# Performance work log

Measured on AMD Instinct MI355X. Metric: run time of the kernel, lower is better.

## Reference

```python
import jax, jax.numpy as jnp
import numpy as np

MARGIN = 0.1
PERM_SEED = 42  # fixed stand-in for torch.randperm per row


def setup_inputs() -> dict:
    key = jax.random.key(0)
    k1, k2, k3 = jax.random.split(key, 3)
    n, d, f = 32768, 1000, 300
    inputs = jax.random.normal(k1, (n, f), dtype=jnp.float32)
    Y = jax.random.normal(k2, (d, f), dtype=jnp.float32)
    y_idxs = jax.random.randint(k3, (n,), 0, d)
    return {"inputs": inputs, "Y": Y, "y_idxs": y_idxs}


def reference(inputs, Y, y_idxs):
    # inputs: [n, f], Y: [d, f] class semantic embeddings, y_idxs: [n]
    n, d = inputs.shape[0], Y.shape[0]

    # All dot products at once: S[i, j] = Y[j] . inputs[i]
    S = inputs @ Y.T  # [n, d]

    # One random class permutation per row (torch.randperm(d) per sample)
    perm_keys = jax.random.split(jax.random.key(PERM_SEED), n)
    perms = jax.vmap(lambda k: jax.random.permutation(k, d))(perm_keys)  # [n, d]

    ap = S[jnp.arange(n), y_idxs]                 # [n]   anchor-positive dots
    an = jnp.take_along_axis(S, perms, axis=1)    # [n, d] anchor-negative dots in perm order

    valid = perms != y_idxs[:, None]              # skip j == y
    # early-break condition at each permutation slot
    cond = valid & ((ap[:, None] - an) > MARGIN)
    c = cond.astype(jnp.int32)
    excl_cum = jnp.cumsum(c, axis=1) - c          # exclusive cumsum of break events
    # include every valid slot up to AND including the first breaking slot
    include = valid & (excl_cum == 0)             # [n, d]

    # MarginRankingLoss with target=1: mean(max(0, margin + an - ap))
    per_pair = jnp.maximum(0.0, MARGIN + an - ap[:, None])
    total = jnp.sum(jnp.where(include, per_pair, 0.0))
    count = jnp.maximum(jnp.sum(include), 1).astype(jnp.float32)
    return total / count
```

## Files before the change

kernel.cpp:

```cpp
#include <hip/hip_runtime.h>
#include <stdint.h>

#define N_ROWS 32768
#define D_CLS  1000
#define D_PAD  1024
#define F_DIM  300
#define F_PAD  320
#define MARGIN 0.1f

#define BM     128
#define BN     128
#define BK     64
#define GTHR   512
#define KGTHR  1024
#define LDTA   328
#define LDTB   72

#define M_PB   32
#define NTHR   512
#define NT_PW  8
#define MT_PB  2
#define LDA    328
#define SROW   34

#define NPART  32

typedef short short8 __attribute__((ext_vector_type(8)));
typedef float f32x4  __attribute__((ext_vector_type(4)));

__device__ __forceinline__ uint32_t rotl32(uint32_t x, int r) {
  return (x << r) | (x >> (32 - r));
}

__device__ __forceinline__ void threefry2x32(uint32_t k0, uint32_t k1,
                                             uint32_t x0, uint32_t x1,
                                             uint32_t& o0, uint32_t& o1) {
  uint32_t k2 = k0 ^ k1 ^ 0x1BD11BDAu;
  x0 += k0; x1 += k1;
#define TF_R(r) { x0 += x1; x1 = rotl32(x1, (r)); x1 ^= x0; }
  TF_R(13) TF_R(15) TF_R(26) TF_R(6)
  x0 += k1; x1 += k2 + 1u;
  TF_R(17) TF_R(29) TF_R(16) TF_R(24)
  x0 += k2; x1 += k0 + 2u;
  TF_R(13) TF_R(15) TF_R(26) TF_R(6)
  x0 += k0; x1 += k1 + 3u;
  TF_R(17) TF_R(29) TF_R(16) TF_R(24)
  x0 += k1; x1 += k2 + 4u;
  TF_R(13) TF_R(15) TF_R(26) TF_R(6)
  x0 += k2; x1 += k0 + 5u;
#undef TF_R
  o0 = x0; o1 = x1;
}

struct TFSched {
  uint32_t k0, k1, k2, k2p1, k0p2, k1p3, k2p4, k0p5;
};
__device__ __forceinline__ TFSched tf_make(uint32_t k0, uint32_t k1) {
  TFSched s;
  s.k0 = k0; s.k1 = k1;
  s.k2 = k0 ^ k1 ^ 0x1BD11BDAu;
  s.k2p1 = s.k2 + 1u; s.k0p2 = k0 + 2u; s.k1p3 = k1 + 3u;
  s.k2p4 = s.k2 + 4u; s.k0p5 = k0 + 5u;
  return s;
}
__device__ __forceinline__ uint32_t tf_hash(const TFSched& s, uint32_t c) {
  uint32_t x0 = s.k0, x1 = c + s.k1;
#define TFH(r) { x0 += x1; x1 = __builtin_amdgcn_alignbit(x1, x1, 32 - (r)); x1 ^= x0; }
  TFH(13) TFH(15) TFH(26) TFH(6)
  x0 += s.k1; x1 += s.k2p1;
  TFH(17) TFH(29) TFH(16) TFH(24)
  x0 += s.k2; x1 += s.k0p2;
  TFH(13) TFH(15) TFH(26) TFH(6)
  x0 += s.k0; x1 += s.k1p3;
  TFH(17) TFH(29) TFH(16) TFH(24)
  x0 += s.k1; x1 += s.k2p4;
  TFH(13) TFH(15) TFH(26) TFH(6)
  x0 += s.k2; x1 += s.k0p5;
#undef TFH
  return x0 ^ x1;
}

__device__ __forceinline__ uint16_t f2bf(float f) {
  uint32_t u = __builtin_bit_cast(uint32_t, f);
  return (uint16_t)((u + 0x7FFFu + ((u >> 16) & 1u)) >> 16);
}
__device__ __forceinline__ float bf2f(uint16_t v) {
  return __builtin_bit_cast(float, (uint32_t)v << 16);
}
__device__ __forceinline__ float bf2f_lo(uint32_t v) {
  return __builtin_bit_cast(float, v << 16);
}
__device__ __forceinline__ float bf2f_hi(uint32_t v) {
  return __builtin_bit_cast(float, v & 0xFFFF0000u);
}

__global__ void prep(const float* __restrict__ Y, uint16_t* __restrict__ Ybf,
                     uint32_t* __restrict__ subk) {
  int i = blockIdx.x * 256 + threadIdx.x;
  if (i < D_PAD * F_PAD) {
    int j = i / F_PAD;
    int k = i - j * F_PAD;
    float v = (j < D_CLS && k < F_DIM) ? Y[j * F_DIM + k] : 0.f;
    Ybf[i] = f2bf(v);
  }
  if (i < N_ROWS) {
    uint32_t r1, r2, s1, s2;
    threefry2x32(0u, 42u, 0u, (uint32_t)i, r1, r2);
    threefry2x32(r1, r2, 0u, 1u, s1, s2);
    subk[2 * i]     = s1;
    subk[2 * i + 1] = s2;
  }
}

__launch_bounds__(KGTHR, 4)
__global__ void gemm_kg(const float* __restrict__ inputs,
                        const uint16_t* __restrict__ Ybf,
                        uint32_t* __restrict__ Spair,
                        uint32_t* __restrict__ keyP,
                        const uint32_t* __restrict__ subk) {
  __shared__ __align__(16) uint16_t A_lds[BM * LDTA];
  __shared__ __align__(16) uint16_t B_lds[2][BN * LDTB];

  const int t    = threadIdx.x;
  const int wave = t >> 6;
  const int lane = t & 63;
  const int l15  = lane & 15;
  const int g    = lane >> 4;
  const bool isg = wave < 8;
  const int wm   = wave >> 1;
  const int wn   = wave & 1;
  const int kw   = wave - 8;
  const int r0   = blockIdx.x * BM;

  for (int i = t; i < BM * (F_DIM / 4); i += KGTHR) {
    int r  = i / 75;
    int c4 = i - r * 75;
    float4 v = *(const float4*)(inputs + (size_t)(r0 + r) * F_DIM + c4 * 4);
    ushort4 o;
    o.x = f2bf(v.x); o.y = f2bf(v.y); o.z = f2bf(v.z); o.w = f2bf(v.w);
    *(ushort4*)&A_lds[r * LDTA + c4 * 4] = o;
  }
  for (int i = t; i < BM * 7; i += KGTHR) {
    int r = i / 7, p = i - r * 7;
    *(ushort4*)&A_lds[r * LDTA + 300 + p * 4] = (ushort4){0, 0, 0, 0};
  }

  const int brow = t >> 3, bkof = t & 7;
  short8 bv[2];
  auto LOADB = [&](int tile) {
    const int c0 = (tile / 5) * BN;
    const int k0 = (tile % 5) * BK;
#pragma unroll
    for (int j = 0; j < 2; ++j)
      bv[j] = *(const short8*)(Ybf + (size_t)(c0 + j * 64 + brow) * F_PAD + k0 + bkof * 8);
  };
  auto WRITEB = [&](int buf) {
#pragma unroll
    for (int j = 0; j < 2; ++j)
      *(short8*)&B_lds[buf][(j * 64 + brow) * LDTB + bkof * 8] = bv[j];
  };

  f32x4 acc[2][4];
#pragma unroll
  for (int mt = 0; mt < 2; ++mt)
#pragma unroll
    for (int nt = 0; nt < 4; ++nt) acc[mt][nt] = (f32x4){0.f, 0.f, 0.f, 0.f};

  if (isg) LOADB(0);
  __syncthreads();
  if (isg) WRITEB(0);
  __syncthreads();

  const int NT = 8 * 5;
#pragma unroll 1
  for (int tile = 0; tile < NT; ++tile) {
    if (isg) {
      const int kt = tile % 5;
      if (tile < NT - 1) LOADB(tile + 1);
      const uint16_t* Bc = B_lds[tile & 1];
#pragma unroll
      for (int ks = 0; ks < 2; ++ks) {
        short8 a[2], b[4];
#pragma unroll
        for (int mt = 0; mt < 2; ++mt)
          a[mt] = *(const short8*)&A_lds[(wm * 32 + mt * 16 + l15) * LDTA + kt * BK + ks * 32 + g * 8];
#pragma unroll
        for (int nt = 0; nt < 4; ++nt)
          b[nt] = *(const short8*)&Bc[(wn * 64 + nt * 16 + l15) * LDTB + ks * 32 + g * 8];
#pragma unroll
        for (int mt = 0; mt < 2; ++mt)
#pragma unroll
          for (int nt = 0; nt < 4; ++nt)
            acc[mt][nt] = __builtin_amdgcn_mfma_f32_16x16x32_bf16(a[mt], b[nt], acc[mt][nt], 0, 0, 0);
      }
      if (kt == 4) {
        const int c0 = (tile / 5) * BN;
#pragma unroll
        for (int mt = 0; mt < 2; ++mt)
#pragma unroll
          for (int nt = 0; nt < 4; ++nt) {
            const int col = c0 + wn * 64 + nt * 16 + l15;
#pragma unroll
            for (int p = 0; p < 2; ++p) {
              uint32_t lo = f2bf(acc[mt][nt][2 * p]);
              uint32_t hi = f2bf(acc[mt][nt][2 * p + 1]);
              size_t rp = (size_t)(r0 >> 1) + wm * 16 + mt * 8 + g * 2 + p;
              Spair[rp * D_PAD + col] = (hi << 16) | lo;
            }
            acc[mt][nt] = (f32x4){0.f, 0.f, 0.f, 0.f};
          }
      }
      if (tile < NT - 1) WRITEB((tile + 1) & 1);
    } else if (tile < 32) {
      const int rp_loc = kw * 8 + (tile >> 2);
      const size_t rpg = (size_t)(r0 >> 1) + rp_loc;
      const int rA = r0 + 2 * rp_loc;
      const uint4 sk4 = *(const uint4*)(subk + 2 * rA);
      const TFSched sA = tf_make(sk4.x, sk4.y);
      const TFSched sB = tf_make(sk4.z, sk4.w);
      const uint32_t c0 = (uint32_t)((tile & 3) * 256 + 4 * lane);
      uint4 ov;
      uint32_t o[4];
#pragma unroll
      for (int j = 0; j < 4; ++j) {
        uint32_t kA = tf_hash(sA, c0 + (uint32_t)j);
        uint32_t kB = tf_hash(sB, c0 + (uint32_t)j);
        o[j] = (kA >> 16) | (kB & 0xFFFF0000u);
      }
      ov.x = o[0]; ov.y = o[1]; ov.z = o[2]; ov.w = o[3];
      *(uint4*)(keyP + (rpg << 10) + c0) = ov;
    }
    if (tile < NT - 1) __syncthreads();
  }
}

__launch_bounds__(256, 4)
__global__ void loss_light(const uint32_t* __restrict__ Spair,
                           const uint32_t* __restrict__ keyP,
                           const int* __restrict__ yidx,
                           float* __restrict__ rowSum,
                           int* __restrict__ rowCnt) {
  const int lane = threadIdx.x & 63;
  const int wave = threadIdx.x >> 6;
  const int rp   = blockIdx.x * 4 + wave;
  const int rA   = 2 * rp;
  const int rB   = rA + 1;
  const int yA = yidx[rA], yB = yidx[rB];
  const uint32_t* Sp = Spair + (size_t)rp * D_PAD;
  const uint32_t* Kp = keyP  + (size_t)rp * D_PAD;
  const float apA = bf2f_lo(Sp[yA]);
  const float apB = bf2f_hi(Sp[yB]);

  uint32_t an[16], kk[16];
#pragma unroll
  for (int q4 = 0; q4 < 4; ++q4) {
    uint4 v = *(const uint4*)(Sp + q4 * 256 + lane * 4);
    an[4 * q4 + 0] = v.x; an[4 * q4 + 1] = v.y;
    an[4 * q4 + 2] = v.z; an[4 * q4 + 3] = v.w;
    uint4 w = *(const uint4*)(Kp + q4 * 256 + lane * 4);
    kk[4 * q4 + 0] = w.x; kk[4 * q4 + 1] = w.y;
    kk[4 * q4 + 2] = w.z; kk[4 * q4 + 3] = w.w;
  }

  uint32_t mnA = 0xFFFFu, mnB = 0xFFFFu;
#pragma unroll
  for (int q = 0; q < 16; ++q) {
    const int c = (q >> 2) * 256 + lane * 4 + (q & 3);
    const uint32_t kA = kk[q] & 0xFFFFu, kB = kk[q] >> 16;
    const float anA = bf2f_lo(an[q]), anB = bf2f_hi(an[q]);
    if ((c < D_CLS) && (c != yA) && (apA - anA) > MARGIN) mnA = (kA < mnA) ? kA : mnA;
    if ((c < D_CLS) && (c != yB) && (apB - anB) > MARGIN) mnB = (kB < mnB) ? kB : mnB;
  }
#pragma unroll
  for (int off = 1; off < 64; off <<= 1) {
    uint32_t oA = __shfl_xor(mnA, off, 64);
    uint32_t oB = __shfl_xor(mnB, off, 64);
    mnA = (oA < mnA) ? oA : mnA;
    mnB = (oB < mnB) ? oB : mnB;
  }

  float smA = 0.f, smB = 0.f; int ctA = 0, ctB = 0;
#pragma unroll
  for (int q = 0; q < 16; ++q) {
    const int c = (q >> 2) * 256 + lane * 4 + (q & 3);
    const uint32_t kA = kk[q] & 0xFFFFu, kB = kk[q] >> 16;
    const float anA = bf2f_lo(an[q]), anB = bf2f_hi(an[q]);
    if ((c < D_CLS) && (c != yA) && kA < mnA) { smA += MARGIN + anA - apA; ctA += 1; }
    if ((c < D_CLS) && (c != yB) && kB < mnB) { smB += MARGIN + anB - apB; ctB += 1; }
  }
#pragma unroll
  for (int off = 1; off < 64; off <<= 1) {
    smA += __shfl_xor(smA, off, 64);
    smB += __shfl_xor(smB, off, 64);
    ctA += __shfl_xor(ctA, off, 64);
    ctB += __shfl_xor(ctB, off, 64);
  }
  if (lane == 0) {
    rowSum[rA] = smA;  rowCnt[rA] = ctA + (mnA != 0xFFFFu ? 1 : 0);
    rowSum[rB] = smB;  rowCnt[rB] = ctB + (mnB != 0xFFFFu ? 1 : 0);
  }
}

__launch_bounds__(GTHR, 1)
__global__ void gemm_s(const float* __restrict__ inputs,
                       const uint16_t* __restrict__ Ybf,
                       uint32_t* __restrict__ Spair) {
  __shared__ __align__(16) uint16_t A_lds[BM * LDTA];
  __shared__ __align__(16) uint16_t B_lds[2][BN * LDTB];

  const int t    = threadIdx.x;
  const int wave = t >> 6;
  const int lane = t & 63;
  const int l15  = lane & 15;
  const int g    = lane >> 4;
  const int wm   = wave >> 1;
  const int wn   = wave & 1;
  const int r0   = blockIdx.x * BM;

  for (int i = t; i < BM * (F_DIM / 4); i += GTHR) {
    int r  = i / 75;
    int c4 = i - r * 75;
    float4 v = *(const float4*)(inputs + (size_t)(r0 + r) * F_DIM + c4 * 4);
    ushort4 o;
    o.x = f2bf(v.x); o.y = f2bf(v.y); o.z = f2bf(v.z); o.w = f2bf(v.w);
    *(ushort4*)&A_lds[r * LDTA + c4 * 4] = o;
  }
  for (int i = t; i < BM * 7; i += GTHR) {
    int r = i / 7, p = i - r * 7;
    *(ushort4*)&A_lds[r * LDTA + 300 + p * 4] = (ushort4){0, 0, 0, 0};
  }

  const int brow = t >> 3, bkof = t & 7;
  short8 bv[2];
  auto LOADB = [&](int tile) {
    const int c0 = (tile / 5) * BN;
    const int k0 = (tile % 5) * BK;
#pragma unroll
    for (int j = 0; j < 2; ++j)
      bv[j] = *(const short8*)(Ybf + (size_t)(c0 + j * 64 + brow) * F_PAD + k0 + bkof * 8);
  };
  auto WRITEB = [&](int buf) {
#pragma unroll
    for (int j = 0; j < 2; ++j)
      *(short8*)&B_lds[buf][(j * 64 + brow) * LDTB + bkof * 8] = bv[j];
  };

  f32x4 acc[2][4];
#pragma unroll
  for (int mt = 0; mt < 2; ++mt)
#pragma unroll
    for (int nt = 0; nt < 4; ++nt) acc[mt][nt] = (f32x4){0.f, 0.f, 0.f, 0.f};

  LOADB(0);
  __syncthreads();
  WRITEB(0);
  __syncthreads();

  const int NT = 8 * 5;
#pragma unroll 1
  for (int tile = 0; tile < NT; ++tile) {
    const int kt = tile % 5;
    if (tile < NT - 1) LOADB(tile + 1);
    const uint16_t* Bc = B_lds[tile & 1];
#pragma unroll
    for (int ks = 0; ks < 2; ++ks) {
      short8 a[2], b[4];
#pragma unroll
      for (int mt = 0; mt < 2; ++mt)
        a[mt] = *(const short8*)&A_lds[(wm * 32 + mt * 16 + l15) * LDTA + kt * BK + ks * 32 + g * 8];
#pragma unroll
      for (int nt = 0; nt < 4; ++nt)
        b[nt] = *(const short8*)&Bc[(wn * 64 + nt * 16 + l15) * LDTB + ks * 32 + g * 8];
#pragma unroll
      for (int mt = 0; mt < 2; ++mt)
#pragma unroll
        for (int nt = 0; nt < 4; ++nt)
          acc[mt][nt] = __builtin_amdgcn_mfma_f32_16x16x32_bf16(a[mt], b[nt], acc[mt][nt], 0, 0, 0);
    }
    if (kt == 4) {
      const int c0 = (tile / 5) * BN;
#pragma unroll
      for (int mt = 0; mt < 2; ++mt)
#pragma unroll
        for (int nt = 0; nt < 4; ++nt) {
          const int col = c0 + wn * 64 + nt * 16 + l15;
#pragma unroll
          for (int p = 0; p < 2; ++p) {
            uint32_t lo = f2bf(acc[mt][nt][2 * p]);
            uint32_t hi = f2bf(acc[mt][nt][2 * p + 1]);
            size_t rp = (size_t)(r0 >> 1) + wm * 16 + mt * 8 + g * 2 + p;
            Spair[rp * D_PAD + col] = (hi << 16) | lo;
          }
          acc[mt][nt] = (f32x4){0.f, 0.f, 0.f, 0.f};
        }
    }
    if (tile < NT - 1) {
      WRITEB((tile + 1) & 1);
      __syncthreads();
    }
  }
}

__launch_bounds__(256, 2)
__global__ void hash_loss(const uint32_t* __restrict__ Spair,
                          const uint32_t* __restrict__ subk,
                          const int* __restrict__ yidx,
                          float* __restrict__ rowSum,
                          int* __restrict__ rowCnt) {
  const int lane = threadIdx.x & 63;
  const int wave = threadIdx.x >> 6;
  const int rp   = blockIdx.x * 4 + wave;
  const int rA   = 2 * rp;
  const int rB   = 2 * rp + 1;

  const int yA = yidx[rA], yB = yidx[rB];
  const TFSched sA = tf_make(subk[2 * rA], subk[2 * rA + 1]);
  const TFSched sB = tf_make(subk[2 * rB], subk[2 * rB + 1]);

  const uint32_t* Sp = Spair + (size_t)rp * D_PAD;
  const float apA = bf2f_lo(Sp[yA]);
  const float apB = bf2f_hi(Sp[yB]);

  uint32_t an[16];
#pragma unroll
  for (int j = 0; j < 4; ++j) {
    uint4 v = *(const uint4*)(Sp + j * 256 + lane * 4);
    an[4 * j + 0] = v.x; an[4 * j + 1] = v.y;
    an[4 * j + 2] = v.z; an[4 * j + 3] = v.w;
  }

  uint32_t skAB[16];
  uint32_t pkA = 0xFFFFFFFFu, pkB = 0xFFFFFFFFu;
#pragma unroll
  for (int q = 0; q < 16; ++q) {
    const int c = (q >> 2) * 256 + lane * 4 + (q & 3);
    uint32_t kA = tf_hash(sA, (uint32_t)c);
    uint32_t kB = tf_hash(sB, (uint32_t)c);
    skAB[q] = (kA >> 16) | (kB & 0xFFFF0000u);
    float anA = bf2f_lo(an[q]);
    float anB = bf2f_hi(an[q]);
    if ((c < D_CLS) && (c != yA) && (apA - anA) > MARGIN) {
      pkA = (kA < pkA) ? kA : pkA;
    }
    if ((c < D_CLS) && (c != yB) && (apB - anB) > MARGIN) {
      pkB = (kB < pkB) ? kB : pkB;
    }
  }
#pragma unroll
  for (int off = 1; off < 64; off <<= 1) {
    uint32_t oA = __shfl_xor(pkA, off, 64);
    uint32_t oB = __shfl_xor(pkB, off, 64);
    pkA = (oA < pkA) ? oA : pkA;
    pkB = (oB < pkB) ? oB : pkB;
  }
  const uint32_t pA16 = pkA >> 16;
  const uint32_t pB16 = pkB >> 16;

  float smA = 0.f, smB = 0.f; int ctA = 0, ctB = 0;
#pragma unroll
  for (int q = 0; q < 16; ++q) {
    const int c = (q >> 2) * 256 + lane * 4 + (q & 3);
    float anA = bf2f_lo(an[q]);
    float anB = bf2f_hi(an[q]);
    if ((c < D_CLS) && (c != yA) && (skAB[q] & 0xFFFFu) < pA16) {
      smA += MARGIN + anA - apA; ctA += 1;
    }
    if ((c < D_CLS) && (c != yB) && (skAB[q] >> 16) < pB16) {
      smB += MARGIN + anB - apB; ctB += 1;
    }
  }
#pragma unroll
  for (int off = 1; off < 64; off <<= 1) {
    smA += __shfl_xor(smA, off, 64);
    smB += __shfl_xor(smB, off, 64);
    ctA += __shfl_xor(ctA, off, 64);
    ctB += __shfl_xor(ctB, off, 64);
  }
  if (lane == 0) {
    rowSum[rA] = smA;
    rowCnt[rA] = ctA + (pkA != 0xFFFFFFFFu ? 1 : 0);
    rowSum[rB] = smB;
    rowCnt[rB] = ctB + (pkB != 0xFFFFFFFFu ? 1 : 0);
  }
}

__launch_bounds__(NTHR, 4)
__global__ void triplet_fused(const float* __restrict__ inputs,
                              const uint16_t* __restrict__ Ybf,
                              const int* __restrict__ yidx,
                              float* __restrict__ rowSum,
                              int* __restrict__ rowCnt) {
  __shared__ __align__(16) uint16_t SH[D_PAD * SROW];
  __shared__ int      y_sh[M_PB];
  __shared__ uint32_t subk_sh[M_PB][2];

  const int t    = threadIdx.x;
  const int wave = t >> 6;
  const int lane = t & 63;
  const int l15  = lane & 15;
  const int g    = lane >> 4;
  const int row0 = blockIdx.x * M_PB;
  const int colbase = wave * (NT_PW * 16);

  if (t < M_PB) {
    y_sh[t] = yidx[row0 + t];
    uint32_t r1, r2, s1, s2;
    threefry2x32(0u, 42u, 0u, (uint32_t)(row0 + t), r1, r2);
    threefry2x32(r1, r2, 0u, 1u, s1, s2);
    subk_sh[t][0] = s1; subk_sh[t][1] = s2;
  }

  uint16_t* A_fl = SH;
  for (int i = t; i < M_PB * (F_DIM / 4); i += NTHR) {
    int r  = i / 75;
    int c4 = i - r * 75;
    float4 v = *(const float4*)(inputs + (size_t)(row0 + r) * F_DIM + c4 * 4);
    ushort4 o;
    o.x = f2bf(v.x); o.y = f2bf(v.y); o.z = f2bf(v.z); o.w = f2bf(v.w);
    *(ushort4*)&A_fl[r * LDA + c4 * 4] = o;
  }
  for (int i = t; i < M_PB * 5; i += NTHR) {
    int r = i / 5, p = i - r * 5;
    *(ushort4*)&A_fl[r * LDA + 300 + p * 4] = (ushort4){0, 0, 0, 0};
  }
  __syncthreads();

  f32x4 acc[MT_PB][NT_PW];
#pragma unroll
  for (int mt = 0; mt < MT_PB; ++mt)
#pragma unroll
    for (int nt = 0; nt < NT_PW; ++nt) acc[mt][nt] = (f32x4){0.f, 0.f, 0.f, 0.f};

  const uint16_t* gB[NT_PW];
#pragma unroll
  for (int nt = 0; nt < NT_PW; ++nt) {
    int j = colbase + nt * 16 + l15;
    gB[nt] = Ybf + (size_t)j * F_PAD + (g << 3);
  }
  const uint16_t* aBase = &A_fl[l15 * LDA + (g << 3)];

#pragma unroll 2
  for (int ks = 0; ks < F_PAD / 32; ++ks) {
    short8 b[NT_PW], a[MT_PB];
#pragma unroll
    for (int nt = 0; nt < NT_PW; ++nt)
      b[nt] = *(const short8*)(gB[nt] + ks * 32);
#pragma unroll
    for (int mt = 0; mt < MT_PB; ++mt)
      a[mt] = *(const short8*)(aBase + mt * 16 * LDA + ks * 32);
#pragma unroll
    for (int mt = 0; mt < MT_PB; ++mt)
#pragma unroll
      for (int nt = 0; nt < NT_PW; ++nt)
        acc[mt][nt] = __builtin_amdgcn_mfma_f32_16x16x32_bf16(a[mt], b[nt], acc[mt][nt], 0, 0, 0);
  }

  __syncthreads();

#pragma unroll
  for (int mt = 0; mt < MT_PB; ++mt)
#pragma unroll
    for (int nt = 0; nt < NT_PW; ++nt) {
      int col = colbase + nt * 16 + l15;
#pragma unroll
      for (int p = 0; p < 2; ++p) {
        uint32_t lo = f2bf(acc[mt][nt][2 * p]);
        uint32_t hi = f2bf(acc[mt][nt][2 * p + 1]);
        *(uint32_t*)&SH[col * SROW + mt * 16 + (g << 2) + 2 * p] = (hi << 16) | lo;
      }
    }
  __syncthreads();

#pragma unroll
  for (int pr = 0; pr < 2; ++pr) {
    const int rA = wave * 4 + pr * 2;
    const int rB = rA + 1;
    const int yA = y_sh[rA], yB = y_sh[rB];
    const uint32_t a1 = subk_sh[rA][0], a2 = subk_sh[rA][1];
    const uint32_t b1 = subk_sh[rB][0], b2 = subk_sh[rB][1];
    const float apA = bf2f(SH[yA * SROW + rA]);
    const float apB = bf2f(SH[yB * SROW + rB]);

    uint32_t skA[16], skB[16];
    uint32_t pkA = 0xFFFFFFFFu, pkB = 0xFFFFFFFFu;
#pragma unroll
    for (int q = 0; q < 16; ++q) {
      const int c = q * 64 + lane;
      uint32_t xA, yAo, xB, yBo;
      threefry2x32(a1, a2, 0u, (uint32_t)c, xA, yAo);
      threefry2x32(b1, b2, 0u, (uint32_t)c, xB, yBo);
      skA[q] = xA ^ yAo;
      skB[q] = xB ^ yBo;
      float anA = bf2f(SH[c * SROW + rA]);
      float anB = bf2f(SH[c * SROW + rB]);
      if ((c < D_CLS) && (c != yA) && (apA - anA) > MARGIN) {
        pkA = (skA[q] < pkA) ? skA[q] : pkA;
      }
      if ((c < D_CLS) && (c != yB) && (apB - anB) > MARGIN) {
        pkB = (skB[q] < pkB) ? skB[q] : pkB;
      }
    }
#pragma unroll
    for (int off = 1; off < 64; off <<= 1) {
      uint32_t oA = __shfl_xor(pkA, off, 64);
      uint32_t oB = __shfl_xor(pkB, off, 64);
      pkA = (oA < pkA) ? oA : pkA;
      pkB = (oB < pkB) ? oB : pkB;
    }
    float smA = 0.f, smB = 0.f; int ctA = 0, ctB = 0;
#pragma unroll
    for (int q = 0; q < 16; ++q) {
      const int c = q * 64 + lane;
      float anA = bf2f(SH[c * SROW + rA]);
      float anB = bf2f(SH[c * SROW + rB]);
      if ((c < D_CLS) && (c != yA) && skA[q] < pkA) { smA += MARGIN + anA - apA; ctA += 1; }
      if ((c < D_CLS) && (c != yB) && skB[q] < pkB) { smB += MARGIN + anB - apB; ctB += 1; }
    }
#pragma unroll
    for (int off = 1; off < 64; off <<= 1) {
      smA += __shfl_xor(smA, off, 64);
      smB += __shfl_xor(smB, off, 64);
      ctA += __shfl_xor(ctA, off, 64);
      ctB += __shfl_xor(ctB, off, 64);
    }
    if (lane == 0) {
      rowSum[row0 + rA] = smA;
      rowCnt[row0 + rA] = ctA + (pkA != 0xFFFFFFFFu ? 1 : 0);
      rowSum[row0 + rB] = smB;
      rowCnt[row0 + rB] = ctB + (pkB != 0xFFFFFFFFu ? 1 : 0);
    }
  }
}

__global__ void reduce_part(const float* __restrict__ rowSum,
                            const int* __restrict__ rowCnt,
                            float* __restrict__ pS, int* __restrict__ pC) {
  __shared__ float ss[4];
  __shared__ int   sc[4];
  const int base = blockIdx.x * (N_ROWS / NPART);
  float s = 0.f; int c = 0;
  for (int i = threadIdx.x; i < N_ROWS / NPART; i += 256) {
    s += rowSum[base + i];
    c += rowCnt[base + i];
  }
#pragma unroll
  for (int off = 32; off > 0; off >>= 1) {
    s += __shfl_down(s, (unsigned)off, 64);
    c += __shfl_down(c, (unsigned)off, 64);
  }
  int wid = threadIdx.x >> 6, lane = threadIdx.x & 63;
  if (lane == 0) { ss[wid] = s; sc[wid] = c; }
  __syncthreads();
  if (threadIdx.x == 0) {
    pS[blockIdx.x] = ss[0] + ss[1] + ss[2] + ss[3];
    pC[blockIdx.x] = sc[0] + sc[1] + sc[2] + sc[3];
  }
}

__global__ void reduce_final(const float* __restrict__ pS,
                             const int* __restrict__ pC,
                             float* __restrict__ out) {
  const int lane = threadIdx.x;
  float s = (lane < NPART) ? pS[lane] : 0.f;
  int   c = (lane < NPART) ? pC[lane] : 0;
#pragma unroll
  for (int off = 32; off > 0; off >>= 1) {
    s += __shfl_down(s, (unsigned)off, 64);
    c += __shfl_down(c, (unsigned)off, 64);
  }
  if (lane == 0) out[0] = s / (float)(c < 1 ? 1 : c);
}

extern "C" void kernel_launch(void* const* d_in, const int* in_sizes, int n_in,
                              void* d_out, int out_size, void* d_ws, size_t ws_size,
                              hipStream_t stream) {
  const float* inputs = (const float*)d_in[0];
  const float* Y      = (const float*)d_in[1];
  const int*   yidx   = (const int*)d_in[2];
  float* out = (float*)d_out;

  char* ws = (char*)d_ws;
  size_t off = 0;
  uint16_t* Ybf    = (uint16_t*)(ws + off); off += (size_t)D_PAD * F_PAD * 2;
  float*    rowSum = (float*)(ws + off);    off += (size_t)N_ROWS * 4;
  int*      rowCnt = (int*)(ws + off);      off += (size_t)N_ROWS * 4;
  uint32_t* subk   = (uint32_t*)(ws + off); off += (size_t)N_ROWS * 8;
  float*    pS     = (float*)(ws + off);    off += (size_t)NPART * 4;
  int*      pC     = (int*)(ws + off);      off += (size_t)NPART * 4;
  off = (off + 255) & ~(size_t)255;
  uint32_t* Spair  = (uint32_t*)(ws + off); off += (size_t)(N_ROWS / 2) * D_PAD * 4;
  const size_t need_mid = off;
  off = (off + 255) & ~(size_t)255;
  uint32_t* keyP   = (uint32_t*)(ws + off); off += (size_t)(N_ROWS / 2) * D_PAD * 4;
  const size_t need_full = off;

  hipLaunchKernelGGL(prep, dim3((D_PAD * F_PAD + 255) / 256), dim3(256),
                     0, stream, Y, Ybf, subk);
  if (ws_size >= need_full) {
    hipLaunchKernelGGL(gemm_kg, dim3(N_ROWS / BM), dim3(KGTHR),
                       0, stream, inputs, Ybf, Spair, keyP, subk);
    hipLaunchKernelGGL(loss_light, dim3(N_ROWS / 8), dim3(256),
                       0, stream, Spair, keyP, yidx, rowSum, rowCnt);
  } else if (ws_size >= need_mid) {
    hipLaunchKernelGGL(gemm_s, dim3(N_ROWS / BM), dim3(GTHR),
                       0, stream, inputs, Ybf, Spair);
    hipLaunchKernelGGL(hash_loss, dim3(N_ROWS / 8), dim3(256),
                       0, stream, Spair, subk, yidx, rowSum, rowCnt);
  } else {
    hipLaunchKernelGGL(triplet_fused, dim3(N_ROWS / M_PB), dim3(NTHR),
                       0, stream, inputs, Ybf, yidx, rowSum, rowCnt);
  }
  hipLaunchKernelGGL(reduce_part, dim3(NPART), dim3(256), 0, stream,
                     rowSum, rowCnt, pS, pC);
  hipLaunchKernelGGL(reduce_final, dim3(1), dim3(64), 0, stream, pS, pC, out);
}
```

Measured before the change: 129.5 us.

## Read B operands directly from global and decouple keygen waves from GEMM barriers

The GEMM waves no longer stage Y tiles in LDS with double-buffered barriers. They load bf16 B fragments straight from global memory (expected to hit L2 because Y is small) and iterate over the full K dimension per column block. The keygen waves now run independently with no per-tile __syncthreads, and the GEMM waves take part of the hash work after their GEMM finishes, which rebalances the load. This removes LDS traffic for B and the barrier coupling between the two roles, at the cost of uncoalesced, global-latency-bound B loads.

```diff
diff --git a/kernel.cpp b/kernel.cpp
--- a/kernel.cpp
+++ b/kernel.cpp
@@ -94,6 +94,29 @@
   return __builtin_bit_cast(float, v & 0xFFFF0000u);
 }
 
+__device__ __forceinline__ void keygen_rp(uint32_t* __restrict__ keyP,
+                                          const uint32_t* __restrict__ subk,
+                                          int r0, int rp_loc, int lane) {
+  const size_t rpg = (size_t)(r0 >> 1) + rp_loc;
+  const int rA = r0 + 2 * rp_loc;
+  const uint4 sk4 = *(const uint4*)(subk + 2 * rA);
+  const TFSched sA = tf_make(sk4.x, sk4.y);
+  const TFSched sB = tf_make(sk4.z, sk4.w);
+#pragma unroll
+  for (int chunk = 0; chunk < 4; ++chunk) {
+    const uint32_t c0 = (uint32_t)(chunk * 256 + 4 * lane);
+    uint32_t o[4];
+#pragma unroll
+    for (int j = 0; j < 4; ++j) {
+      uint32_t kA = tf_hash(sA, c0 + (uint32_t)j);
+      uint32_t kB = tf_hash(sB, c0 + (uint32_t)j);
+      o[j] = (kA >> 16) | (kB & 0xFFFF0000u);
+    }
+    uint4 ov; ov.x = o[0]; ov.y = o[1]; ov.z = o[2]; ov.w = o[3];
+    *(uint4*)(keyP + (rpg << 10) + c0) = ov;
+  }
+}
+
 __global__ void prep(const float* __restrict__ Y, uint16_t* __restrict__ Ybf,
                      uint32_t* __restrict__ subk) {
   int i = blockIdx.x * 256 + threadIdx.x;
@@ -113,23 +136,18 @@
 }
 
 __launch_bounds__(KGTHR, 4)
-__global__ void gemm_kg(const float* __restrict__ inputs,
-                        const uint16_t* __restrict__ Ybf,
-                        uint32_t* __restrict__ Spair,
-                        uint32_t* __restrict__ keyP,
-                        const uint32_t* __restrict__ subk) {
+__global__ void gk2(const float* __restrict__ inputs,
+                    const uint16_t* __restrict__ Ybf,
+                    uint32_t* __restrict__ Spair,
+                    uint32_t* __restrict__ keyP,
+                    const uint32_t* __restrict__ subk) {
   __shared__ __align__(16) uint16_t A_lds[BM * LDTA];
-  __shared__ __align__(16) uint16_t B_lds[2][BN * LDTB];
 
   const int t    = threadIdx.x;
   const int wave = t >> 6;
   const int lane = t & 63;
   const int l15  = lane & 15;
   const int g    = lane >> 4;
-  const bool isg = wave < 8;
-  const int wm   = wave >> 1;
-  const int wn   = wave & 1;
-  const int kw   = wave - 8;
   const int r0   = blockIdx.x * BM;
 
   for (int i = t; i < BM * (F_DIM / 4); i += KGTHR) {
@@ -144,93 +162,66 @@
     int r = i / 7, p = i - r * 7;
     *(ushort4*)&A_lds[r * LDTA + 300 + p * 4] = (ushort4){0, 0, 0, 0};
   }
-
-  const int brow = t >> 3, bkof = t & 7;
-  short8 bv[2];
-  auto LOADB = [&](int tile) {
-    const int c0 = (tile / 5) * BN;
-    const int k0 = (tile % 5) * BK;
-#pragma unroll
-    for (int j = 0; j < 2; ++j)
-      bv[j] = *(const short8*)(Ybf + (size_t)(c0 + j * 64 + brow) * F_PAD + k0 + bkof * 8);
-  };
-  auto WRITEB = [&](int buf) {
-#pragma unroll
-    for (int j = 0; j < 2; ++j)
-      *(short8*)&B_lds[buf][(j * 64 + brow) * LDTB + bkof * 8] = bv[j];
-  };
-
-  f32x4 acc[2][4];
-#pragma unroll
-  for (int mt = 0; mt < 2; ++mt)
-#pragma unroll
-    for (int nt = 0; nt < 4; ++nt) acc[mt][nt] = (f32x4){0.f, 0.f, 0.f, 0.f};
-
-  if (isg) LOADB(0);
   __syncthreads();
-  if (isg) WRITEB(0);
-  __syncthreads();
-
-  const int NT = 8 * 5;
+
+  if (wave < 8) {
+    const int wm = wave >> 1;
+    const int wn = wave & 1;
+    const uint16_t* aBase = &A_lds[(wm * 32 + l15) * LDTA + g * 8];
+
 #pragma unroll 1
-  for (int tile = 0; tile < NT; ++tile) {
-    if (isg) {
-      const int kt = tile % 5;
-      if (tile < NT - 1) LOADB(tile + 1);
-      const uint16_t* Bc = B_lds[tile & 1];
-#pragma unroll
-      for (int ks = 0; ks < 2; ++ks) {
+    for (int cn = 0; cn < 8; ++cn) {
+      f32x4 acc[2][4];
+#pragma unroll
+      for (int mt = 0; mt < 2; ++mt)
+#pragma unroll
+        for (int nt = 0; nt < 4; ++nt) acc[mt][nt] = (f32x4){0.f, 0.f, 0.f, 0.f};
+
+      const uint16_t* gB[4];
+#pragma unroll
+      for (int nt = 0; nt < 4; ++nt) {
+        const int col = cn * 128 + wn * 64 + nt * 16 + l15;
+        gB[nt] = Ybf + (size_t)col * F_PAD + g * 8;
+      }
+
+#pragma unroll 2
+      for (int ks = 0; ks < F_PAD / 32; ++ks) {
         short8 a[2], b[4];
 #pragma unroll
+        for (int nt = 0; nt < 4; ++nt)
+          b[nt] = *(const short8*)(gB[nt] + ks * 32);
+#pragma unroll
         for (int mt = 0; mt < 2; ++mt)
-          a[mt] = *(const short8*)&A_lds[(wm * 32 + mt * 16 + l15) * LDTA + kt * BK + ks * 32 + g * 8];
-#pragma unroll
-        for (int nt = 0; nt < 4; ++nt)
-          b[nt] = *(const short8*)&Bc[(wn * 64 + nt * 16 + l15) * LDTB + ks * 32 + g * 8];
+          a[mt] = *(const short8*)(aBase + mt * 16 * LDTA + ks * 32);
 #pragma unroll
         for (int mt = 0; mt < 2; ++mt)
 #pragma unroll
           for (int nt = 0; nt < 4; ++nt)
             acc[mt][nt] = __builtin_amdgcn_mfma_f32_16x16x32_bf16(a[mt], b[nt], acc[mt][nt], 0, 0, 0);
       }
-      if (kt == 4) {
-        const int c0 = (tile / 5) * BN;
-#pragma unroll
-        for (int mt = 0; mt < 2; ++mt)
-#pragma unroll
-          for (int nt = 0; nt < 4; ++nt) {
-            const int col = c0 + wn * 64 + nt * 16 + l15;
-#pragma unroll
-            for (int p = 0; p < 2; ++p) {
-              uint32_t lo = f2bf(acc[mt][nt][2 * p]);
-              uint32_t hi = f2bf(acc[mt][nt][2 * p + 1]);
-              size_t rp = (size_t)(r0 >> 1) + wm * 16 + mt * 8 + g * 2 + p;
-              Spair[rp * D_PAD + col] = (hi << 16) | lo;
-            }
-            acc[mt][nt] = (f32x4){0.f, 0.f, 0.f, 0.f};
+
+#pragma unroll
+      for (int mt = 0; mt < 2; ++mt)
+#pragma unroll
+        for (int nt = 0; nt < 4; ++nt) {
+          const int col = cn * 128 + wn * 64 + nt * 16 + l15;
+#pragma unroll
+          for (int p = 0; p < 2; ++p) {
+            uint32_t lo = f2bf(acc[mt][nt][2 * p]);
+            uint32_t hi = f2bf(acc[mt][nt][2 * p + 1]);
+            size_t rp = (size_t)(r0 >> 1) + wm * 16 + mt * 8 + g * 2 + p;
+            Spair[rp * D_PAD + col] = (hi << 16) | lo;
           }
-      }
-      if (tile < NT - 1) WRITEB((tile + 1) & 1);
-    } else if (tile < 32) {
-      const int rp_loc = kw * 8 + (tile >> 2);
-      const size_t rpg = (size_t)(r0 >> 1) + rp_loc;
-      const int rA = r0 + 2 * rp_loc;
-      const uint4 sk4 = *(const uint4*)(subk + 2 * rA);
-      const TFSched sA = tf_make(sk4.x, sk4.y);
-      const TFSched sB = tf_make(sk4.z, sk4.w);
-      const uint32_t c0 = (uint32_t)((tile & 3) * 256 + 4 * lane);
-      uint4 ov;
-      uint32_t o[4];
-#pragma unroll
-      for (int j = 0; j < 4; ++j) {
-        uint32_t kA = tf_hash(sA, c0 + (uint32_t)j);
-        uint32_t kB = tf_hash(sB, c0 + (uint32_t)j);
-        o[j] = (kA >> 16) | (kB & 0xFFFF0000u);
-      }
-      ov.x = o[0]; ov.y = o[1]; ov.z = o[2]; ov.w = o[3];
-      *(uint4*)(keyP + (rpg << 10) + c0) = ov;
-    }
-    if (tile < NT - 1) __syncthreads();
+        }
+    }
+#pragma unroll 1
+    for (int i = 0; i < 2; ++i)
+      keygen_rp(keyP, subk, r0, 48 + wave * 2 + i, lane);
+  } else {
+    const int kw = wave - 8;
+#pragma unroll 1
+    for (int i = 0; i < 6; ++i)
+      keygen_rp(keyP, subk, r0, kw * 6 + i, lane);
   }
 }
 
@@ -697,7 +688,7 @@
   hipLaunchKernelGGL(prep, dim3((D_PAD * F_PAD + 255) / 256), dim3(256),
                      0, stream, Y, Ybf, subk);
   if (ws_size >= need_full) {
-    hipLaunchKernelGGL(gemm_kg, dim3(N_ROWS / BM), dim3(KGTHR),
+    hipLaunchKernelGGL(gk2, dim3(N_ROWS / BM), dim3(KGTHR),
                        0, stream, inputs, Ybf, Spair, keyP, subk);
     hipLaunchKernelGGL(loss_light, dim3(N_ROWS / 8), dim3(256),
                        0, stream, Spair, keyP, yidx, rowSum, rowCnt);
```

Measured after the change: 133.0 us. +2.7%, slower.
